# Optimization experiments

Measured on AMD Instinct MI355X. Metric: run time of the kernel, lower is better.

The kernel has to match this reference:

```python
import jax, jax.numpy as jnp
from jax import lax
import numpy as np

B, FRAMES, H, W = 8, 128, 64, 64
N_MFCC = 60
VID_FEAT = 196
D = VID_FEAT + N_MFCC   # COMBINE_SIZE = 256
ED = 2 * D              # mamba d_inner = 512
NST = 16                # d_state
DTR = 16                # dt_rank = ceil(D/16)
NL = 4                  # layers per direction
NC = 2                  # num_classes


def setup_inputs() -> dict:
    key = jax.random.key(0)
    ks = iter(jax.random.split(key, 64))
    def rn(shape, s=0.02):
        return jax.random.normal(next(ks), shape, jnp.float32) * s
    inp = {
        'video_input': jax.random.normal(next(ks), (B, FRAMES, 3, H, W), jnp.float32),
        'audio_input': jax.random.normal(next(ks), (B, FRAMES * N_MFCC), jnp.float32),
        'cnn_conv1_w': rn((32, 3, 3, 3), 0.1), 'cnn_conv1_b': jnp.zeros((32,), jnp.float32),
        'cnn_conv2_w': rn((64, 32, 3, 3), 0.05), 'cnn_conv2_b': jnp.zeros((64,), jnp.float32),
        'cnn_fc_w': rn((VID_FEAT, 64), 0.1), 'cnn_fc_b': jnp.zeros((VID_FEAT,), jnp.float32),
    }
    for pref in ('fwd', 'bwd'):
        inp[pref + '_norm_w'] = jnp.ones((NL, D), jnp.float32)
        inp[pref + '_in_proj_w'] = rn((NL, 2 * ED, D))
        inp[pref + '_conv_w'] = rn((NL, ED, 4), 0.1)
        inp[pref + '_conv_b'] = jnp.zeros((NL, ED), jnp.float32)
        inp[pref + '_x_proj_w'] = rn((NL, DTR + 2 * NST, ED))
        inp[pref + '_dt_w'] = rn((NL, ED, DTR), 0.1)
        inp[pref + '_dt_b'] = jnp.zeros((NL, ED), jnp.float32)
        inp[pref + '_A_log'] = jnp.tile(jnp.log(jnp.arange(1, NST + 1, dtype=jnp.float32)), (NL, ED, 1))
        inp[pref + '_D'] = jnp.ones((NL, ED), jnp.float32)
        inp[pref + '_out_proj_w'] = rn((NL, D, ED))
    inp['fc_w'] = rn((D, 2 * D)); inp['fc_b'] = jnp.zeros((D,), jnp.float32)
    inp['fc2_w'] = rn((NC, D)); inp['fc2_b'] = jnp.zeros((NC,), jnp.float32)
    return inp


def _rmsnorm(x, w, eps=1e-5):
    return x * lax.rsqrt(jnp.mean(x * x, -1, keepdims=True) + eps) * w


def _conv2d(x, w, b):
    y = lax.conv_general_dilated(x, w, (1, 1), 'SAME', dimension_numbers=('NCHW', 'OIHW', 'NCHW'))
    return y + b[None, :, None, None]


def _maxpool2(x):
    return lax.reduce_window(x, -jnp.inf, lax.max, (1, 1, 2, 2), (1, 1, 2, 2), 'VALID')


def _video_cnn(x, w1, b1, w2, b2, fw, fb):
    x = _maxpool2(jax.nn.relu(_conv2d(x, w1, b1)))
    x = _maxpool2(jax.nn.relu(_conv2d(x, w2, b2)))
    x = jnp.mean(x, (2, 3))            # global avg pool -> [B*F, 64]
    return x @ fw.T + fb               # [B*F, VID_FEAT]


def _mamba_layer(x, norm_w, in_w, conv_w, conv_b, xp_w, dt_w, dt_b, A_log, Dp, out_w):
    Bsz, L, _ = x.shape
    xn = _rmsnorm(x, norm_w)
    xz = jnp.einsum('bld,ed->ble', xn, in_w)        # [B,L,2*ED]
    xc, z = jnp.split(xz, 2, axis=-1)
    # causal depthwise conv1d, kernel 4
    xpad = jnp.pad(xc, ((0, 0), (3, 0), (0, 0)))
    xc = sum(xpad[:, k:k + L, :] * conv_w[:, k] for k in range(4)) + conv_b
    xc = jax.nn.silu(xc)
    dbc = jnp.einsum('ble,re->blr', xc, xp_w)       # [B,L,DTR+2*NST]
    dt, Bm, Cm = dbc[..., :DTR], dbc[..., DTR:DTR + NST], dbc[..., DTR + NST:]
    delta = jax.nn.softplus(jnp.einsum('blr,er->ble', dt, dt_w) + dt_b)  # [B,L,ED]
    A = -jnp.exp(A_log)                             # [ED,NST]
    dA = jnp.exp(delta[..., None] * A)              # [B,L,ED,NST]
    dBx = delta[..., None] * Bm[:, :, None, :] * xc[..., None]
    def step(h, inp):
        dA_t, dBx_t, c_t = inp
        h = dA_t * h + dBx_t
        return h, jnp.einsum('ben,bn->be', h, c_t)
    h0 = jnp.zeros((Bsz, ED, NST), x.dtype)
    _, ys = lax.scan(step, h0, (dA.transpose(1, 0, 2, 3), dBx.transpose(1, 0, 2, 3), Cm.transpose(1, 0, 2)))
    y = ys.transpose(1, 0, 2) + Dp * xc
    y = y * jax.nn.silu(z)
    return x + jnp.einsum('ble,de->bld', y, out_w)


def _mamba(x, norm_w, in_w, conv_w, conv_b, xp_w, dt_w, dt_b, A_log, Dp, out_w):
    for l in range(NL):
        x = _mamba_layer(x, norm_w[l], in_w[l], conv_w[l], conv_b[l], xp_w[l],
                         dt_w[l], dt_b[l], A_log[l], Dp[l], out_w[l])
    return x


def reference(video_input, audio_input, cnn_conv1_w, cnn_conv1_b, cnn_conv2_w, cnn_conv2_b,
              cnn_fc_w, cnn_fc_b,
              fwd_norm_w, fwd_in_proj_w, fwd_conv_w, fwd_conv_b, fwd_x_proj_w, fwd_dt_w,
              fwd_dt_b, fwd_A_log, fwd_D, fwd_out_proj_w,
              bwd_norm_w, bwd_in_proj_w, bwd_conv_w, bwd_conv_b, bwd_x_proj_w, bwd_dt_w,
              bwd_dt_b, bwd_A_log, bwd_D, bwd_out_proj_w,
              fc_w, fc_b, fc2_w, fc2_b):
    bsz, frames = video_input.shape[0], video_input.shape[1]
    xv = video_input.reshape(bsz * frames, 3, H, W)
    xv = _video_cnn(xv, cnn_conv1_w, cnn_conv1_b, cnn_conv2_w, cnn_conv2_b, cnn_fc_w, cnn_fc_b)
    xv = xv.reshape(bsz, frames, VID_FEAT)
    xa = audio_input.reshape(bsz, -1, N_MFCC)       # [B, frames, N_MFCC]
    xc = jnp.concatenate([xv, xa], axis=-1)         # [B, frames, D]
    xf = _mamba(xc, fwd_norm_w, fwd_in_proj_w, fwd_conv_w, fwd_conv_b, fwd_x_proj_w,
                fwd_dt_w, fwd_dt_b, fwd_A_log, fwd_D, fwd_out_proj_w)
    xb = _mamba(xc[:, ::-1], bwd_norm_w, bwd_in_proj_w, bwd_conv_w, bwd_conv_b, bwd_x_proj_w,
                bwd_dt_w, bwd_dt_b, bwd_A_log, bwd_D, bwd_out_proj_w)[:, ::-1]
    x_last = jnp.concatenate([xf, xb], axis=-1)[:, -1, :]   # [B, 2*D]; dropout = identity (eval)
    x = x_last @ fc_w.T + fc_b
    return x @ fc2_w.T + fc2_b
```

## Files before the change

kernel.cpp:

```cpp
#include <hip/hip_runtime.h>
#include <hip/hip_bf16.h>
#include <cstdint>
#include <cstddef>

#define BATCH 8
#define FRAMES 128
#define TOK (BATCH*FRAMES)
#define NM 60
#define VF 196
#define DD 256
#define EDIM 512
#define NSTATE 16
#define DTRANK 16
#define NLAYER 4

typedef __attribute__((ext_vector_type(8))) short short8v;
typedef __attribute__((ext_vector_type(4))) float f32x4;

__device__ __forceinline__ unsigned short f2bf(float f) {
  unsigned x = __float_as_uint(f);
  unsigned r = (x + 0x7FFFu + ((x >> 16) & 1u)) >> 16;
  return (unsigned short)r;
}

__global__ void pack_w2(const float* __restrict__ w2, unsigned short* __restrict__ Wb,
                        const float* __restrict__ w1, unsigned short* __restrict__ Wb1) {
  int id = blockIdx.x * 256 + threadIdx.x;
  if (id < 9 * 4 * 64) {
    int lane = id & 63;
    int mt = (id >> 6) & 3;
    int sh = id >> 8;
    int dy = sh / 3, dx = sh % 3;
    int oc = mt * 16 + (lane & 15);
    int ic0 = (lane >> 4) * 8;
    unsigned u[4];
#pragma unroll
    for (int p = 0; p < 4; ++p) {
      unsigned short lo = f2bf(w2[((oc * 32 + ic0 + 2 * p) * 3 + dy) * 3 + dx]);
      unsigned short hi = f2bf(w2[((oc * 32 + ic0 + 2 * p + 1) * 3 + dy) * 3 + dx]);
      u[p] = (unsigned)lo | ((unsigned)hi << 16);
    }
    uint4 v = {u[0], u[1], u[2], u[3]};
    *(uint4*)(Wb + (size_t)id * 8) = v;
  } else if (id < 9 * 4 * 64 + 128) {
    int id2 = id - 9 * 4 * 64;
    int mt = id2 >> 6, lane = id2 & 63;
    int oc = mt * 16 + (lane & 15);
    int ko = lane >> 4;
    unsigned u[4];
#pragma unroll
    for (int p = 0; p < 4; ++p) {
      int k0 = ko * 8 + 2 * p, k1 = k0 + 1;
      unsigned short lo = (k0 < 27) ? f2bf(w1[oc * 27 + k0]) : 0;
      unsigned short hi = (k1 < 27) ? f2bf(w1[oc * 27 + k1]) : 0;
      u[p] = (unsigned)lo | ((unsigned)hi << 16);
    }
    uint4 v = {u[0], u[1], u[2], u[3]};
    *(uint4*)(Wb1 + (size_t)id2 * 8) = v;
  }
}

__global__ void pack_mamba(const float* __restrict__ ipF, const float* __restrict__ ipR,
                           const float* __restrict__ opF, const float* __restrict__ opR,
                           const float* __restrict__ xpF, const float* __restrict__ xpR,
                           unsigned short* __restrict__ Wip, unsigned short* __restrict__ Wop,
                           unsigned short* __restrict__ Wxp) {
  int id = blockIdx.x * 256 + threadIdx.x;
  if (id < 262144) {
    int dl = id >> 15, r = id & 32767;
    int ntile = r >> 9, kt = (r >> 6) & 7, lane = r & 63;
    int dir = dl >> 2, layer = dl & 3;
    const float* src = (dir ? ipR : ipF) + (size_t)layer * 1024 * 256
                       + (size_t)(ntile * 16 + (lane & 15)) * 256 + kt * 32 + (lane >> 4) * 8;
    unsigned u[4];
#pragma unroll
    for (int p = 0; p < 4; ++p)
      u[p] = (unsigned)f2bf(src[2 * p]) | ((unsigned)f2bf(src[2 * p + 1]) << 16);
    uint4 v = {u[0], u[1], u[2], u[3]};
    *(uint4*)(Wip + (size_t)id * 8) = v;
  } else if (id < 262144 + 131072) {
    int id2 = id - 262144;
    int dl = id2 >> 14, rr = id2 & 16383;
    int ntile = rr >> 10, kt = (rr >> 6) & 15, lane = rr & 63;
    int dir = dl >> 2, layer = dl & 3;
    const float* src = (dir ? opR : opF) + (size_t)layer * 256 * 512
                       + (size_t)(ntile * 16 + (lane & 15)) * 512 + kt * 32 + (lane >> 4) * 8;
    unsigned u[4];
#pragma unroll
    for (int p = 0; p < 4; ++p)
      u[p] = (unsigned)f2bf(src[2 * p]) | ((unsigned)f2bf(src[2 * p + 1]) << 16);
    uint4 v = {u[0], u[1], u[2], u[3]};
    *(uint4*)(Wop + (size_t)id2 * 8) = v;
  } else if (id < 262144 + 131072 + 24576) {
    int id3 = id - 262144 - 131072;
    int dl = id3 / 3072, rr = id3 % 3072;
    int ntile = rr >> 10, kt = (rr >> 6) & 15, lane = rr & 63;
    int dir = dl >> 2, layer = dl & 3;
    const float* src = (dir ? xpR : xpF) + (size_t)layer * 48 * 512
                       + (size_t)(ntile * 16 + (lane & 15)) * 512 + kt * 32 + (lane >> 4) * 8;
    unsigned u[4];
#pragma unroll
    for (int p = 0; p < 4; ++p)
      u[p] = (unsigned)f2bf(src[2 * p]) | ((unsigned)f2bf(src[2 * p + 1]) << 16);
    uint4 v = {u[0], u[1], u[2], u[3]};
    *(uint4*)(Wxp + (size_t)id3 * 8) = v;
  }
}

#define C1RS 68
#define C1ICS (66*68)
__global__ __launch_bounds__(256) void conv1_mfma(
    const float* __restrict__ video, const unsigned short* __restrict__ Wb1,
    const float* __restrict__ b1, unsigned short* __restrict__ X1)
{
  __shared__ unsigned short ldsu[3 * C1ICS + 96];
  const int img = blockIdx.x, t = threadIdx.x;
  const float* vin = video + (size_t)img * 12288;
  const int lane = t & 63, wv = t >> 6;
  const int col = lane & 15, ko = lane >> 4;

  for (int i = t; i < (3 * C1ICS + 96) / 2; i += 256) ((unsigned*)ldsu)[i] = 0;
  __syncthreads();
#pragma unroll
  for (int i = 0; i < 12; ++i) {
    int c = i * 256 + t;
    int ic = c >> 10, rem = c & 1023, gy = rem >> 4, c4 = rem & 15;
    float4 v = *(const float4*)(vin + ic * 4096 + gy * 64 + c4 * 4);
    unsigned lo = (unsigned)f2bf(v.x) | ((unsigned)f2bf(v.y) << 16);
    unsigned hi = (unsigned)f2bf(v.z) | ((unsigned)f2bf(v.w) << 16);
    int di = ic * C1ICS + (gy + 1) * C1RS + 4 + c4 * 4;
    *(uint2*)(ldsu + di) = (uint2){lo, hi};
  }

  short8v A0 = *(const short8v*)(Wb1 + (size_t)(0 * 64 + lane) * 8);
  short8v A1 = *(const short8v*)(Wb1 + (size_t)(1 * 64 + lane) * 8);
  float bia[2][4];
#pragma unroll
  for (int mt = 0; mt < 2; ++mt)
#pragma unroll
    for (int r = 0; r < 4; ++r) bia[mt][r] = b1[mt * 16 + ko * 4 + r];

  int offs[8];
#pragma unroll
  for (int j = 0; j < 8; ++j) {
    int k = ko * 8 + j;
    int o = 0;
    if (k < 27) {
      int ic = k / 9, tap = k - ic * 9;
      int dy = tap / 3, dx = tap - dy * 3;
      o = ic * C1ICS + dy * C1RS + dx + 3;
    }
    offs[j] = o;
  }
  __syncthreads();

  f32x4 z4 = {0.f, 0.f, 0.f, 0.f};
#pragma unroll 1
  for (int rp = 0; rp < 8; ++rp) {
    const int y0 = wv * 16 + rp * 2;
#pragma unroll
    for (int xg = 0; xg < 4; ++xg) {
      const int bse = y0 * C1RS + xg * 16 + col;
      short8v vb0, vb1;
#pragma unroll
      for (int j = 0; j < 8; ++j) {
        vb0[j] = (short)ldsu[bse + offs[j]];
        vb1[j] = (short)ldsu[bse + C1RS + offs[j]];
      }
      f32x4 c00 = __builtin_amdgcn_mfma_f32_16x16x32_bf16(A0, vb0, z4, 0, 0, 0);
      f32x4 c10 = __builtin_amdgcn_mfma_f32_16x16x32_bf16(A1, vb0, z4, 0, 0, 0);
      f32x4 c01 = __builtin_amdgcn_mfma_f32_16x16x32_bf16(A0, vb1, z4, 0, 0, 0);
      f32x4 c11 = __builtin_amdgcn_mfma_f32_16x16x32_bf16(A1, vb1, z4, 0, 0, 0);
      const int py = wv * 8 + rp;
      const int pxp = xg * 8 + (col >> 1);
#pragma unroll
      for (int mt = 0; mt < 2; ++mt) {
        f32x4 ca = mt ? c10 : c00;
        f32x4 cb = mt ? c11 : c01;
        unsigned pk[2];
#pragma unroll
        for (int r = 0; r < 4; ++r) {
          float va = fmaxf(ca[r] + bia[mt][r], 0.f);
          float vb = fmaxf(cb[r] + bia[mt][r], 0.f);
          float v = fmaxf(va, vb);
          v = fmaxf(v, __shfl_xor(v, 1, 64));
          unsigned short u = f2bf(v);
          if ((r & 1) == 0) pk[r >> 1] = (unsigned)u;
          else              pk[r >> 1] |= ((unsigned)u << 16);
        }
        if ((col & 1) == 0) {
          uint2 o = {pk[0], pk[1]};
          *(uint2*)(X1 + ((size_t)(img * 1024 + py * 32 + pxp) * 32 + mt * 16 + ko * 4)) = o;
        }
      }
    }
  }
}

#define X_LDS_BYTES (4 * 1156 * 16)
#define OCT_STRIDE  (1156 * 16)
__global__ __launch_bounds__(256) void conv2_k(
    const unsigned short* __restrict__ X1, const unsigned short* __restrict__ Wb,
    const float* __restrict__ b2, float* __restrict__ feat)
{
  extern __shared__ char sm[];
  float* part = (float*)(sm + X_LDS_BYTES);
  const int img = blockIdx.x, t = threadIdx.x;
  const int lane = t & 63, wv = t >> 6;
  const int kg = lane >> 4, l15 = lane & 15;

  for (int j = t; j < 1156; j += 256) {
    int r = j / 34, cc = j - r * 34;
    if (r == 0 || r == 33 || cc == 0 || cc == 33) {
      uint4 z = {0, 0, 0, 0};
#pragma unroll
      for (int oct = 0; oct < 4; ++oct)
        *(uint4*)(sm + oct * OCT_STRIDE + j * 16) = z;
    }
  }
  const uint4* src = (const uint4*)(X1 + (size_t)img * 32768);
#pragma unroll 4
  for (int i = 0; i < 16; ++i) {
    int c = i * 256 + t;
    uint4 v = src[c];
    int oct = c & 3, P = c >> 2;
    int y = P >> 5, x = P & 31;
    *(uint4*)(sm + oct * OCT_STRIDE + ((y + 1) * 34 + (x + 1)) * 16) = v;
  }
  __syncthreads();

  float bia[4][4];
#pragma unroll
  for (int mt = 0; mt < 4; ++mt)
#pragma unroll
    for (int r = 0; r < 4; ++r) bia[mt][r] = b2[mt * 16 + kg * 4 + r];

  float msum[4][4];
#pragma unroll
  for (int mt = 0; mt < 4; ++mt)
#pragma unroll
    for (int r = 0; r < 4; ++r) msum[mt][r] = 0.f;

#pragma unroll 1
  for (int pass = 0; pass < 2; ++pass) {
    f32x4 acc[4][8];
#pragma unroll
    for (int mt = 0; mt < 4; ++mt)
#pragma unroll
      for (int q = 0; q < 8; ++q) acc[mt][q] = (f32x4){0.f, 0.f, 0.f, 0.f};
    int Pq[8];
#pragma unroll
    for (int q = 0; q < 8; ++q) {
      int p = (wv * 16 + pass * 8 + q) * 16 + l15;
      int y = p >> 5, x = p & 31;
      Pq[q] = y * 34 + x;
    }
#pragma unroll
    for (int sh = 0; sh < 9; ++sh) {
      const int dy = sh / 3, dx = sh % 3;
      const int shoff = (dy * 34 + dx) * 16;
      short8v Af[4];
#pragma unroll
      for (int mt = 0; mt < 4; ++mt)
        Af[mt] = *(const short8v*)(Wb + ((size_t)(sh * 4 + mt) * 64 + lane) * 8);
#pragma unroll
      for (int q = 0; q < 8; ++q) {
        short8v Bf = *(const short8v*)(sm + kg * OCT_STRIDE + Pq[q] * 16 + shoff);
#pragma unroll
        for (int mt = 0; mt < 4; ++mt)
          acc[mt][q] = __builtin_amdgcn_mfma_f32_16x16x32_bf16(Af[mt], Bf, acc[mt][q], 0, 0, 0);
      }
    }
#pragma unroll
    for (int mt = 0; mt < 4; ++mt) {
#pragma unroll
      for (int pr = 0; pr < 4; ++pr) {
        int qa = (pr & 1) + (pr >> 1) * 4;
        int qb = qa + 2;
#pragma unroll
        for (int r = 0; r < 4; ++r) {
          float va = fmaxf(acc[mt][qa][r] + bia[mt][r], 0.f);
          float vb = fmaxf(acc[mt][qb][r] + bia[mt][r], 0.f);
          float v = fmaxf(va, vb);
          v = fmaxf(v, __shfl_xor(v, 1, 64));
          msum[mt][r] += v;
        }
      }
    }
  }
#pragma unroll
  for (int mt = 0; mt < 4; ++mt)
#pragma unroll
    for (int r = 0; r < 4; ++r) {
      float v = msum[mt][r];
      v += __shfl_xor(v, 1, 64);
      v += __shfl_xor(v, 2, 64);
      v += __shfl_xor(v, 4, 64);
      v += __shfl_xor(v, 8, 64);
      if (l15 == 0) part[wv * 64 + mt * 16 + kg * 4 + r] = v * 0.5f;
    }
  __syncthreads();
  if (t < 64)
    feat[(size_t)img * 64 + t] =
        (part[t] + part[64 + t] + part[128 + t] + part[192 + t]) * (1.f / 256.f);
}

__global__ __launch_bounds__(256) void fcgemm_k(
    const float* __restrict__ A, const float* __restrict__ B,
    const float* __restrict__ bias, float* __restrict__ xf, float* __restrict__ xr)
{
  __shared__ float sA[16][68];
  __shared__ float sB[16][68];
  const int t = threadIdx.x;
  const int m0 = blockIdx.x * 64;
  const int n0 = blockIdx.y * 64;
  const int tx = t & 15, ty = t >> 4;
  const int lk = t & 15, lr = t >> 4;
  float acc[4][4] = {};
  for (int k0 = 0; k0 < 64; k0 += 16) {
#pragma unroll
    for (int rr = 0; rr < 4; ++rr) {
      int m = m0 + lr + rr * 16;
      sA[lk][lr + rr * 16] = A[(size_t)m * 64 + k0 + lk];
      int n = n0 + lr + rr * 16;
      sB[lk][lr + rr * 16] = (n < VF) ? B[(size_t)n * 64 + k0 + lk] : 0.f;
    }
    __syncthreads();
#pragma unroll
    for (int kk = 0; kk < 16; ++kk) {
      float a0 = sA[kk][ty*4+0], a1 = sA[kk][ty*4+1], a2 = sA[kk][ty*4+2], a3 = sA[kk][ty*4+3];
      float b0 = sB[kk][tx*4+0], b1 = sB[kk][tx*4+1], b2 = sB[kk][tx*4+2], b3 = sB[kk][tx*4+3];
      acc[0][0]=fmaf(a0,b0,acc[0][0]); acc[0][1]=fmaf(a0,b1,acc[0][1]); acc[0][2]=fmaf(a0,b2,acc[0][2]); acc[0][3]=fmaf(a0,b3,acc[0][3]);
      acc[1][0]=fmaf(a1,b0,acc[1][0]); acc[1][1]=fmaf(a1,b1,acc[1][1]); acc[1][2]=fmaf(a1,b2,acc[1][2]); acc[1][3]=fmaf(a1,b3,acc[1][3]);
      acc[2][0]=fmaf(a2,b0,acc[2][0]); acc[2][1]=fmaf(a2,b1,acc[2][1]); acc[2][2]=fmaf(a2,b2,acc[2][2]); acc[2][3]=fmaf(a2,b3,acc[2][3]);
      acc[3][0]=fmaf(a3,b0,acc[3][0]); acc[3][1]=fmaf(a3,b1,acc[3][1]); acc[3][2]=fmaf(a3,b2,acc[3][2]); acc[3][3]=fmaf(a3,b3,acc[3][3]);
    }
    __syncthreads();
  }
#pragma unroll
  for (int i = 0; i < 4; ++i) {
    int m = m0 + ty * 4 + i;
    int b = m >> 7, l = m & 127;
    int mr = (b << 7) + (127 - l);
#pragma unroll
    for (int j = 0; j < 4; ++j) {
      int n = n0 + tx * 4 + j;
      if (n >= VF) continue;
      float v = acc[i][j] + bias[n];
      xf[(size_t)m * DD + n] = v;
      xr[(size_t)mr * DD + n] = v;
    }
  }
}

__global__ void audio_k(const float* __restrict__ audio,
                        float* __restrict__ xf, float* __restrict__ xr) {
  int i = blockIdx.x * 256 + threadIdx.x;
  if (i >= BATCH * FRAMES * NM) return;
  int j = i % NM; int l = (i / NM) % FRAMES; int b = i / (NM * FRAMES);
  float v = audio[i];
  xf[(size_t)(b * FRAMES + l) * DD + VF + j] = v;
  xr[(size_t)(b * FRAMES + (FRAMES - 1 - l)) * DD + VF + j] = v;
}

__global__ __launch_bounds__(256) void inproj_mfma3(
    const float* __restrict__ xF, const float* __restrict__ xR,
    const float* __restrict__ nwF, const float* __restrict__ nwR,
    const unsigned short* __restrict__ Wip, int layer,
    float* __restrict__ xzF, float* __restrict__ xzR)
{
  const int dir = blockIdx.z;
  const float* x = dir ? xR : xF;
  const float* nw = dir ? nwR : nwF;
  float* xz = dir ? xzR : xzF;
  __shared__ unsigned short sa[32 * 16 * 8];
  const int t = threadIdx.x;
  const int tok0 = blockIdx.x * 16;
  {
    const int tk = t >> 4, l16 = t & 15;
    const float* row = x + (size_t)(tok0 + tk) * DD + l16 * 16;
    float v[16];
    float ss = 0.f;
#pragma unroll
    for (int i = 0; i < 4; ++i) {
      float4 f = ((const float4*)row)[i];
      v[4*i] = f.x; v[4*i+1] = f.y; v[4*i+2] = f.z; v[4*i+3] = f.w;
      ss += f.x*f.x + f.y*f.y + f.z*f.z + f.w*f.w;
    }
    ss += __shfl_xor(ss, 1, 16);
    ss += __shfl_xor(ss, 2, 16);
    ss += __shfl_xor(ss, 4, 16);
    ss += __shfl_xor(ss, 8, 16);
    float scale = rsqrtf(ss * (1.f / DD) + 1e-5f);
    const float* nwp = nw + l16 * 16;
#pragma unroll
    for (int hh = 0; hh < 2; ++hh) {
      unsigned ub[4];
#pragma unroll
      for (int p = 0; p < 4; ++p) {
        unsigned short lo = f2bf(v[hh*8 + 2*p]     * scale * nwp[hh*8 + 2*p]);
        unsigned short hi = f2bf(v[hh*8 + 2*p + 1] * scale * nwp[hh*8 + 2*p + 1]);
        ub[p] = (unsigned)lo | ((unsigned)hi << 16);
      }
      int k0 = l16 * 16 + hh * 8;
      int kt = k0 >> 5, oct = (k0 >> 3) & 3;
      uint4 w4 = {ub[0], ub[1], ub[2], ub[3]};
      *(uint4*)(sa + ((size_t)(kt * 4 + oct) * 16 + tk) * 8) = w4;
    }
  }
  __syncthreads();
  const int lane = t & 63, w = t >> 6;
  short8v af[8];
#pragma unroll
  for (int kt = 0; kt < 8; ++kt)
    af[kt] = *(const short8v*)(sa + ((size_t)(kt * 4 + (lane >> 4)) * 16 + (lane & 15)) * 8);
#pragma unroll
  for (int ns = 0; ns < 4; ++ns) {
    const int ntile = blockIdx.y * 16 + w * 4 + ns;
    const unsigned short* wb = Wip + (((size_t)(dir * 4 + layer) * 512 + ntile * 8) * 64 + lane) * 8;
    f32x4 acc = (f32x4){0.f, 0.f, 0.f, 0.f};
#pragma unroll
    for (int kt = 0; kt < 8; ++kt) {
      short8v bf = *(const short8v*)(wb + (size_t)kt * 64 * 8);
      acc = __builtin_amdgcn_mfma_f32_16x16x32_bf16(af[kt], bf, acc, 0, 0, 0);
    }
#pragma unroll
    for (int r = 0; r < 4; ++r)
      xz[(size_t)(tok0 + (lane >> 4) * 4 + r) * 1024 + ntile * 16 + (lane & 15)] = acc[r];
  }
}

__global__ __launch_bounds__(256) void convsilu2_k(
    const float* __restrict__ xzF, const float* __restrict__ xzR,
    const float* __restrict__ cwF, const float* __restrict__ cwR,
    const float* __restrict__ cbF, const float* __restrict__ cbR,
    float* __restrict__ xcF, float* __restrict__ xcR,
    unsigned short* __restrict__ xcbF, unsigned short* __restrict__ xcbR)
{
  const int dir = blockIdx.z;
  const float* xz = dir ? xzR : xzF;
  const float* cw = dir ? cwR : cwF;
  const float* cb = dir ? cbR : cbF;
  float* xc = dir ? xcR : xcF;
  unsigned short* xcb = dir ? xcbR : xcbF;

  int i = blockIdx.x * 256 + threadIdx.x;
  int tok = i >> 6;
  int e0 = (i & 63) << 3;
  int l = tok & 127;
  const float* col = xz + (size_t)tok * 1024 + e0;

  float v3[8] = {}, v2[8] = {}, v1[8] = {}, v0[8];
  if (l >= 3) { *(float4*)v3 = *(const float4*)(col - 3072); *(float4*)(v3+4) = *(const float4*)(col - 3068); }
  if (l >= 2) { *(float4*)v2 = *(const float4*)(col - 2048); *(float4*)(v2+4) = *(const float4*)(col - 2044); }
  if (l >= 1) { *(float4*)v1 = *(const float4*)(col - 1024); *(float4*)(v1+4) = *(const float4*)(col - 1020); }
  *(float4*)v0 = *(const float4*)col; *(float4*)(v0+4) = *(const float4*)(col + 4);

  float cbv[8];
  *(float4*)cbv = *(const float4*)(cb + e0); *(float4*)(cbv+4) = *(const float4*)(cb + e0 + 4);

  float res[8];
#pragma unroll
  for (int j = 0; j < 8; ++j) {
    float4 cv = ((const float4*)cw)[e0 + j];
    float a = cbv[j];
    a = fmaf(cv.x, v3[j], a);
    a = fmaf(cv.y, v2[j], a);
    a = fmaf(cv.z, v1[j], a);
    a = fmaf(cv.w, v0[j], a);
    res[j] = a / (1.f + __expf(-a));
  }
  float4 r0 = {res[0], res[1], res[2], res[3]};
  float4 r1 = {res[4], res[5], res[6], res[7]};
  float* xcp = xc + (size_t)tok * EDIM + e0;
  *(float4*)xcp = r0; *(float4*)(xcp + 4) = r1;

  unsigned ub[4];
#pragma unroll
  for (int p = 0; p < 4; ++p)
    ub[p] = (unsigned)f2bf(res[2*p]) | ((unsigned)f2bf(res[2*p+1]) << 16);
  int kt = e0 >> 5, oct = (e0 >> 3) & 3;
  uint4 w4 = {ub[0], ub[1], ub[2], ub[3]};
  *(uint4*)(xcb + ((size_t)(kt * 4 + oct) * 1024 + tok) * 8) = w4;
}

__global__ __launch_bounds__(64) void xproj_mfma(
    const unsigned short* __restrict__ xcbF, const unsigned short* __restrict__ xcbR,
    const unsigned short* __restrict__ Wxp, int layer,
    float* __restrict__ dbF, float* __restrict__ dbR)
{
  const int dir = blockIdx.z;
  const unsigned short* xcb = dir ? xcbR : xcbF;
  float* db = dir ? dbR : dbF;
  const int lane = threadIdx.x & 63;
  const int tok0 = blockIdx.x * 16;
  const unsigned short* wbase = Wxp + ((size_t)(dir * 4 + layer) * 3 * 16 * 64) * 8;
  f32x4 acc[3];
#pragma unroll
  for (int nt = 0; nt < 3; ++nt) acc[nt] = (f32x4){0.f, 0.f, 0.f, 0.f};
#pragma unroll
  for (int kt = 0; kt < 16; ++kt) {
    short8v af = *(const short8v*)(xcb + ((size_t)(kt * 4 + (lane >> 4)) * 1024 + tok0 + (lane & 15)) * 8);
#pragma unroll
    for (int nt = 0; nt < 3; ++nt) {
      short8v bf = *(const short8v*)(wbase + ((size_t)(nt * 16 + kt) * 64 + lane) * 8);
      acc[nt] = __builtin_amdgcn_mfma_f32_16x16x32_bf16(af, bf, acc[nt], 0, 0, 0);
    }
  }
#pragma unroll
  for (int nt = 0; nt < 3; ++nt)
#pragma unroll
    for (int r = 0; r < 4; ++r)
      db[(size_t)(tok0 + (lane >> 4) * 4 + r) * 48 + nt * 16 + (lane & 15)] = acc[nt][r];
}

__global__ __launch_bounds__(256) void scan4_k(
    const float* __restrict__ xzF, const float* __restrict__ xzR,
    const float* __restrict__ xcF, const float* __restrict__ xcR,
    const float* __restrict__ dbF, const float* __restrict__ dbR,
    const float* __restrict__ dwF, const float* __restrict__ dwR,
    const float* __restrict__ dtbF, const float* __restrict__ dtbR,
    const float* __restrict__ AlF, const float* __restrict__ AlR,
    const float* __restrict__ DpF, const float* __restrict__ DpR,
    unsigned short* __restrict__ yoF, unsigned short* __restrict__ yoR)
{
  const int dir = blockIdx.z;
  const float* xz = dir ? xzR : xzF;
  const float* xc = dir ? xcR : xcF;
  const float* db = dir ? dbR : dbF;
  const float* dw = dir ? dwR : dwF;
  const float* dtbv = dir ? dtbR : dtbF;
  const float* Al = dir ? AlR : AlF;
  const float* Dp = dir ? DpR : DpF;
  unsigned short* yo = dir ? yoR : yoF;

  __shared__ float sdb[FRAMES * 48];
  __shared__ float sxc[FRAMES * 16];
  __shared__ float sgz[FRAMES * 16];
  __shared__ float sdl[FRAMES * 16];
  const int b = blockIdx.x >> 5;
  const int e0 = (blockIdx.x & 31) << 4;
  const int t = threadIdx.x, g = t >> 4, n = t & 15;
  const int e = e0 + g;

  const float* dbp = db + (size_t)b * FRAMES * 48;
  for (int i = t; i < FRAMES * 48 / 4; i += 256)
    ((float4*)sdb)[i] = ((const float4*)dbp)[i];
  for (int i = t; i < FRAMES * 16; i += 256) {
    int l = i >> 4, c = i & 15;
    int ee = e0 + c;
    sxc[i] = xc[(size_t)(b * FRAMES + l) * EDIM + ee];
    float zz = xz[(size_t)(b * FRAMES + l) * 1024 + 512 + ee];
    sgz[i] = zz / (1.f + __expf(-zz));
    const float* d = db + (size_t)(b * FRAMES + l) * 48;
    const float* w = dw + (size_t)ee * 16;
    float a = dtbv[ee];
#pragma unroll
    for (int q = 0; q < 4; ++q) {
      float4 dv = *(const float4*)(d + 4 * q);
      float4 wv = *(const float4*)(w + 4 * q);
      a = fmaf(dv.x, wv.x, a); a = fmaf(dv.y, wv.y, a);
      a = fmaf(dv.z, wv.z, a); a = fmaf(dv.w, wv.w, a);
    }
    sdl[i] = (a > 20.f) ? a : __logf(1.f + __expf(a));
  }
  float An = -expf(Al[e * NSTATE + n]);
  float Dv = Dp[e];
  float h = 0.f;
  unsigned short* yp = yo + ((size_t)((e >> 5) * 4 + ((e >> 3) & 3)) * 1024 + b * FRAMES) * 8 + (e & 7);
  __syncthreads();

#pragma unroll 1
  for (int l = 0; l < FRAMES; ++l) {
    float dlt = sdl[l * 16 + g];
    float xcv = sxc[l * 16 + g];
    float Bn = sdb[l * 48 + 16 + n];
    float Cn = sdb[l * 48 + 32 + n];
    float dA = __expf(dlt * An);
    h = fmaf(dA, h, dlt * xcv * Bn);
    float part = h * Cn;
    part += __shfl_xor(part, 1, 16);
    part += __shfl_xor(part, 2, 16);
    part += __shfl_xor(part, 4, 16);
    part += __shfl_xor(part, 8, 16);
    if (n == 0) {
      float a2 = fmaf(Dv, xcv, part);
      yp[(size_t)l * 8] = f2bf(a2 * sgz[l * 16 + g]);
    }
  }
}

__global__ __launch_bounds__(256) void outproj_mfma(
    const unsigned short* __restrict__ yoF, const unsigned short* __restrict__ yoR,
    const unsigned short* __restrict__ Wop, int layer,
    float* __restrict__ xF, float* __restrict__ xR)
{
  const int dir = blockIdx.z;
  const unsigned short* yo = dir ? yoR : yoF;
  float* xx = dir ? xR : xF;
  const int t = threadIdx.x, lane = t & 63, w = t >> 6;
  const int m0 = blockIdx.x * 32, n0 = blockIdx.y * 64;
  const int ntile = blockIdx.y * 4 + w;
  const unsigned short* wb = Wop + (((size_t)(dir * 4 + layer) * 256 + ntile * 16) * 64 + lane) * 8;
  f32x4 acc[2];
  acc[0] = (f32x4){0.f, 0.f, 0.f, 0.f};
  acc[1] = (f32x4){0.f, 0.f, 0.f, 0.f};
#pragma unroll
  for (int kt = 0; kt < 16; ++kt) {
    short8v bf = *(const short8v*)(wb + (size_t)kt * 64 * 8);
#pragma unroll
    for (int mt = 0; mt < 2; ++mt) {
      short8v af = *(const short8v*)(yo + ((size_t)(kt * 4 + (lane >> 4)) * 1024 + m0 + mt * 16 + (lane & 15)) * 8);
      acc[mt] = __builtin_amdgcn_mfma_f32_16x16x32_bf16(af, bf, acc[mt], 0, 0, 0);
    }
  }
#pragma unroll
  for (int mt = 0; mt < 2; ++mt)
#pragma unroll
    for (int r = 0; r < 4; ++r) {
      size_t ci = (size_t)(m0 + mt * 16 + (lane >> 4) * 4 + r) * DD + n0 + w * 16 + (lane & 15);
      xx[ci] += acc[mt][r];
    }
}

__global__ __launch_bounds__(256) void head_k(
    const float* __restrict__ xf, const float* __restrict__ xr,
    const float* __restrict__ fcw, const float* __restrict__ fcb,
    const float* __restrict__ fc2w, const float* __restrict__ fc2b,
    float* __restrict__ out)
{
  int b = blockIdx.x;
  __shared__ float xl[2 * DD];
  __shared__ float h[DD];
  __shared__ float hp[4];
  int t = threadIdx.x;
  xl[t]      = xf[(size_t)(b * FRAMES + FRAMES - 1) * DD + t];
  xl[DD + t] = xr[(size_t)(b * FRAMES + 0) * DD + t];
  __syncthreads();
  float acc = fcb[t];
  for (int k = 0; k < 2 * DD; ++k) acc = fmaf(xl[k], fcw[(size_t)t * 2 * DD + k], acc);
  h[t] = acc;
  __syncthreads();
  {
    int c = t >> 7, k = t & 127;
    float p = h[k] * fc2w[c * DD + k] + h[k + 128] * fc2w[c * DD + k + 128];
#pragma unroll
    for (int off = 32; off; off >>= 1) p += __shfl_xor(p, off, 64);
    if ((t & 63) == 0) hp[t >> 6] = p;
  }
  __syncthreads();
  if (t < 2) out[b * 2 + t] = hp[2 * t] + hp[2 * t + 1] + fc2b[t];
}

extern "C" void kernel_launch(void* const* d_in, const int* in_sizes, int n_in,
                              void* d_out, int out_size, void* d_ws, size_t ws_size,
                              hipStream_t stream) {
  const float* video = (const float*)d_in[0];
  const float* audio = (const float*)d_in[1];
  const float* c1w = (const float*)d_in[2];
  const float* c1b = (const float*)d_in[3];
  const float* c2w = (const float*)d_in[4];
  const float* c2b = (const float*)d_in[5];
  const float* fcw = (const float*)d_in[6];
  const float* fcb = (const float*)d_in[7];
  const float* Wf[10]; const float* Wb_[10];
  for (int i = 0; i < 10; ++i) { Wf[i] = (const float*)d_in[8+i]; Wb_[i] = (const float*)d_in[18+i]; }
  const float* fc_w  = (const float*)d_in[28];
  const float* fc_b  = (const float*)d_in[29];
  const float* fc2_w = (const float*)d_in[30];
  const float* fc2_b = (const float*)d_in[31];
  float* out = (float*)d_out;

  float* ws   = (float*)d_ws;
  float* feat = ws;
  float* xf   = feat + 65536;
  float* xr   = xf   + 262144;
  float* xzF  = xr   + 262144;
  float* xzR  = xzF  + 1048576;
  float* xcF  = xzR  + 1048576;
  float* xcR  = xcF  + 524288;
  float* dbF  = xcR  + 524288;
  float* dbR  = dbF  + 49152;
  unsigned short* yoF = (unsigned short*)(dbR + 49152);
  unsigned short* yoR = yoF + 524288;
  unsigned short* X1  = yoR + 524288;
  unsigned short* Wbp = X1 + 33554432;
  unsigned short* Wip = Wbp + 18432;
  unsigned short* Wop = Wip + 2097152;
  unsigned short* Wxp = Wop + 1048576;
  unsigned short* xcbF = Wxp + 196608;
  unsigned short* xcbR = xcbF + 524288;
  unsigned short* Wb1  = xcbR + 524288;

  pack_w2<<<dim3(10), 256, 0, stream>>>(c2w, Wbp, c1w, Wb1);
  pack_mamba<<<dim3(1632), 256, 0, stream>>>(Wf[1], Wb_[1], Wf[9], Wb_[9], Wf[4], Wb_[4],
                                             Wip, Wop, Wxp);
  conv1_mfma<<<dim3(TOK), 256, 0, stream>>>(video, Wb1, c1b, X1);
  conv2_k<<<dim3(TOK), 256, (size_t)(X_LDS_BYTES + 1024), stream>>>(X1, Wbp, c2b, feat);

  fcgemm_k<<<dim3(16, 4), 256, 0, stream>>>(feat, fcw, fcb, xf, xr);
  audio_k<<<dim3((BATCH*FRAMES*NM + 255)/256), 256, 0, stream>>>(audio, xf, xr);

  for (int l = 0; l < NLAYER; ++l) {
    const float* nwF  = Wf[0] + l*DD;              const float* nwR  = Wb_[0] + l*DD;
    const float* cwF_ = Wf[2] + l*EDIM*4;          const float* cwR_ = Wb_[2] + l*EDIM*4;
    const float* cbF_ = Wf[3] + l*EDIM;            const float* cbR_ = Wb_[3] + l*EDIM;
    const float* dwF  = Wf[5] + l*EDIM*DTRANK;     const float* dwR  = Wb_[5] + l*EDIM*DTRANK;
    const float* dtbF = Wf[6] + l*EDIM;            const float* dtbR = Wb_[6] + l*EDIM;
    const float* AlF  = Wf[7] + l*EDIM*NSTATE;     const float* AlR  = Wb_[7] + l*EDIM*NSTATE;
    const float* DpF  = Wf[8] + l*EDIM;            const float* DpR  = Wb_[8] + l*EDIM;

    inproj_mfma3<<<dim3(64, 4, 2), 256, 0, stream>>>(xf, xr, nwF, nwR, Wip, l, xzF, xzR);
    convsilu2_k<<<dim3(256, 1, 2), 256, 0, stream>>>(xzF, xzR, cwF_, cwR_, cbF_, cbR_,
                                                     xcF, xcR, xcbF, xcbR);
    xproj_mfma<<<dim3(64, 1, 2), 64, 0, stream>>>(xcbF, xcbR, Wxp, l, dbF, dbR);
    scan4_k<<<dim3(256, 1, 2), 256, 0, stream>>>(xzF, xzR, xcF, xcR, dbF, dbR, dwF, dwR,
                                                 dtbF, dtbR, AlF, AlR, DpF, DpR, yoF, yoR);
    outproj_mfma<<<dim3(32, 4, 2), 256, 0, stream>>>(yoF, yoR, Wop, l, xf, xr);
  }

  head_k<<<dim3(BATCH), 256, 0, stream>>>(xf, xr, fc_w, fc_b, fc2_w, fc2_b, out);
}
```

Before: 385.2 us.

## Write padded conv1 output to global and read conv2 operands directly from global

conv1 now writes its pooled bf16 output into a zero-bordered 34x34 padded layout in global memory, including the zero halo. conv2 drops its LDS staging of the input image and loads MFMA B fragments straight from global (L2/L1), freeing about 74KB of LDS per block to raise occupancy. Passes are split from 2x8 to 4x4 tiles to lower register pressure. The trade-off is that the nine shifted re-reads per pixel go through the cache hierarchy instead of LDS, and the larger padded buffer adds some global write traffic.

```diff
diff --git a/kernel.cpp b/kernel.cpp
--- a/kernel.cpp
+++ b/kernel.cpp
@@ -109,6 +109,7 @@
 
 #define C1RS 68
 #define C1ICS (66*68)
+#define X1PIX 1156
 __global__ __launch_bounds__(256) void conv1_mfma(
     const float* __restrict__ video, const unsigned short* __restrict__ Wb1,
     const float* __restrict__ b1, unsigned short* __restrict__ X1)
@@ -118,6 +119,18 @@
   const float* vin = video + (size_t)img * 12288;
   const int lane = t & 63, wv = t >> 6;
   const int col = lane & 15, ko = lane >> 4;
+  unsigned short* xout = X1 + (size_t)img * (X1PIX * 32);
+
+  for (int j = t; j < 132; j += 256) {
+    int y, x;
+    if (j < 34)       { y = 0;       x = j; }
+    else if (j < 68)  { y = 33;      x = j - 34; }
+    else if (j < 100) { y = j - 67;  x = 0; }
+    else              { y = j - 99;  x = 33; }
+    uint4 z = {0, 0, 0, 0};
+    uint4* p = (uint4*)(xout + ((size_t)y * 34 + x) * 32);
+    p[0] = z; p[1] = z; p[2] = z; p[3] = z;
+  }
 
   for (int i = t; i < (3 * C1ICS + 96) / 2; i += 256) ((unsigned*)ldsu)[i] = 0;
   __syncthreads();
@@ -190,44 +203,22 @@
         }
         if ((col & 1) == 0) {
           uint2 o = {pk[0], pk[1]};
-          *(uint2*)(X1 + ((size_t)(img * 1024 + py * 32 + pxp) * 32 + mt * 16 + ko * 4)) = o;
+          *(uint2*)(xout + (((size_t)(py + 1) * 34 + (pxp + 1)) * 32 + mt * 16 + ko * 4)) = o;
         }
       }
     }
   }
 }
 
-#define X_LDS_BYTES (4 * 1156 * 16)
-#define OCT_STRIDE  (1156 * 16)
 __global__ __launch_bounds__(256) void conv2_k(
     const unsigned short* __restrict__ X1, const unsigned short* __restrict__ Wb,
     const float* __restrict__ b2, float* __restrict__ feat)
 {
-  extern __shared__ char sm[];
-  float* part = (float*)(sm + X_LDS_BYTES);
+  __shared__ float part[256];
   const int img = blockIdx.x, t = threadIdx.x;
   const int lane = t & 63, wv = t >> 6;
   const int kg = lane >> 4, l15 = lane & 15;
-
-  for (int j = t; j < 1156; j += 256) {
-    int r = j / 34, cc = j - r * 34;
-    if (r == 0 || r == 33 || cc == 0 || cc == 33) {
-      uint4 z = {0, 0, 0, 0};
-#pragma unroll
-      for (int oct = 0; oct < 4; ++oct)
-        *(uint4*)(sm + oct * OCT_STRIDE + j * 16) = z;
-    }
-  }
-  const uint4* src = (const uint4*)(X1 + (size_t)img * 32768);
-#pragma unroll 4
-  for (int i = 0; i < 16; ++i) {
-    int c = i * 256 + t;
-    uint4 v = src[c];
-    int oct = c & 3, P = c >> 2;
-    int y = P >> 5, x = P & 31;
-    *(uint4*)(sm + oct * OCT_STRIDE + ((y + 1) * 34 + (x + 1)) * 16) = v;
-  }
-  __syncthreads();
+  const unsigned short* xim = X1 + (size_t)img * (X1PIX * 32);
 
   float bia[4][4];
 #pragma unroll
@@ -242,30 +233,30 @@
     for (int r = 0; r < 4; ++r) msum[mt][r] = 0.f;
 
 #pragma unroll 1
-  for (int pass = 0; pass < 2; ++pass) {
-    f32x4 acc[4][8];
+  for (int pass = 0; pass < 4; ++pass) {
+    f32x4 acc[4][4];
 #pragma unroll
     for (int mt = 0; mt < 4; ++mt)
 #pragma unroll
-      for (int q = 0; q < 8; ++q) acc[mt][q] = (f32x4){0.f, 0.f, 0.f, 0.f};
-    int Pq[8];
-#pragma unroll
-    for (int q = 0; q < 8; ++q) {
-      int p = (wv * 16 + pass * 8 + q) * 16 + l15;
+      for (int q = 0; q < 4; ++q) acc[mt][q] = (f32x4){0.f, 0.f, 0.f, 0.f};
+    int Pq[4];
+#pragma unroll
+    for (int q = 0; q < 4; ++q) {
+      int p = (wv * 16 + pass * 4 + q) * 16 + l15;
       int y = p >> 5, x = p & 31;
-      Pq[q] = y * 34 + x;
+      Pq[q] = (y * 34 + x) * 32;
     }
 #pragma unroll
     for (int sh = 0; sh < 9; ++sh) {
       const int dy = sh / 3, dx = sh % 3;
-      const int shoff = (dy * 34 + dx) * 16;
+      const int shoff = (dy * 34 + dx) * 32 + kg * 8;
       short8v Af[4];
 #pragma unroll
       for (int mt = 0; mt < 4; ++mt)
         Af[mt] = *(const short8v*)(Wb + ((size_t)(sh * 4 + mt) * 64 + lane) * 8);
 #pragma unroll
-      for (int q = 0; q < 8; ++q) {
-        short8v Bf = *(const short8v*)(sm + kg * OCT_STRIDE + Pq[q] * 16 + shoff);
+      for (int q = 0; q < 4; ++q) {
+        short8v Bf = *(const short8v*)(xim + Pq[q] + shoff);
 #pragma unroll
         for (int mt = 0; mt < 4; ++mt)
           acc[mt][q] = __builtin_amdgcn_mfma_f32_16x16x32_bf16(Af[mt], Bf, acc[mt][q], 0, 0, 0);
@@ -274,9 +265,8 @@
 #pragma unroll
     for (int mt = 0; mt < 4; ++mt) {
 #pragma unroll
-      for (int pr = 0; pr < 4; ++pr) {
-        int qa = (pr & 1) + (pr >> 1) * 4;
-        int qb = qa + 2;
+      for (int pr = 0; pr < 2; ++pr) {
+        int qa = pr, qb = pr + 2;
 #pragma unroll
         for (int r = 0; r < 4; ++r) {
           float va = fmaxf(acc[mt][qa][r] + bia[mt][r], 0.f);
@@ -684,7 +674,7 @@
   unsigned short* yoF = (unsigned short*)(dbR + 49152);
   unsigned short* yoR = yoF + 524288;
   unsigned short* X1  = yoR + 524288;
-  unsigned short* Wbp = X1 + 33554432;
+  unsigned short* Wbp = X1 + 37879808;
   unsigned short* Wip = Wbp + 18432;
   unsigned short* Wop = Wip + 2097152;
   unsigned short* Wxp = Wop + 1048576;
@@ -696,7 +686,7 @@
   pack_mamba<<<dim3(1632), 256, 0, stream>>>(Wf[1], Wb_[1], Wf[9], Wb_[9], Wf[4], Wb_[4],
                                              Wip, Wop, Wxp);
   conv1_mfma<<<dim3(TOK), 256, 0, stream>>>(video, Wb1, c1b, X1);
-  conv2_k<<<dim3(TOK), 256, (size_t)(X_LDS_BYTES + 1024), stream>>>(X1, Wbp, c2b, feat);
+  conv2_k<<<dim3(TOK), 256, 0, stream>>>(X1, Wbp, c2b, feat);
 
   fcgemm_k<<<dim3(16, 4), 256, 0, stream>>>(feat, fcw, fcb, xf, xr);
   audio_k<<<dim3((BATCH*FRAMES*NM + 255)/256), 256, 0, stream>>>(audio, xf, xr);
```

Result: slower. 404.8 us (+5.1%).
